# Performance work log

Hardware: AMD Instinct MI355X
Metric: run time of the kernel (lower is better)

The kernel has to match this reference:

```python
import jax, jax.numpy as jnp
import numpy as np
import math

B, S, D, H = 2, 2048, 1024, 16
HD = D // H  # head_dim = 64

def setup_inputs() -> dict:
    key = jax.random.key(0)
    ks = jax.random.split(key, 11)
    def n(k, shape, scale=1.0):
        return jax.random.normal(k, shape, dtype=jnp.float32) * scale
    w_scale = 1.0 / math.sqrt(D)
    return {
        "q": n(ks[0], (B, S, D)),
        "k": n(ks[1], (B, S, D)),
        "v": n(ks[2], (B, S, D)),
        "WQ_w": n(ks[3], (D, D), w_scale),
        "WQ_b": n(ks[4], (D,), 0.01),
        "WK_w": n(ks[5], (D, D), w_scale),
        "WK_b": n(ks[6], (D,), 0.01),
        "WV_w": n(ks[7], (D, D), w_scale),
        "WV_b": n(ks[8], (D,), 0.01),
        "Wout_w": n(ks[9], (D, D), w_scale),
        "Wout_b": n(ks[10], (D,), 0.01),
    }

def reference(q, k, v, WQ_w, WQ_b, WK_w, WK_b, WV_w, WV_b, Wout_w, Wout_b):
    b, s, _ = k.shape
    # QKV projections (torch Linear: x @ W.T + b; here weights stored [in, out])
    qh = (q @ WQ_w + WQ_b).reshape(b, -1, H, HD).transpose(0, 2, 1, 3)  # [b,h,s,hd]
    kh = (k @ WK_w + WK_b).reshape(b, -1, H, HD).transpose(0, 2, 1, 3)
    vh = (v @ WV_w + WV_b).reshape(b, -1, H, HD).transpose(0, 2, 1, 3)
    # naive attention: full [b,h,s,s] score matrix
    scores = jnp.einsum("bhqd,bhkd->bhqk", qh, kh) / math.sqrt(HD)
    attn = jax.nn.softmax(scores, axis=-1)
    out = jnp.einsum("bhqk,bhkd->bhqd", attn, vh)
    concat = out.transpose(0, 2, 1, 3).reshape(b, -1, H * HD)  # [b,s,inner_dim]
    return concat @ Wout_w + Wout_b
```

## Files before the change

kernel.cpp:

```cpp
#include <hip/hip_runtime.h>
#include <hip/hip_bf16.h>
#include <stdint.h>

typedef __attribute__((ext_vector_type(8))) short bf16x8;
typedef __attribute__((ext_vector_type(4))) short short4v;
typedef __attribute__((ext_vector_type(4))) float f32x4;

#define MFMA16x16x32 __builtin_amdgcn_mfma_f32_16x16x32_bf16

__device__ __forceinline__ short f2b(float f) {
  union { float f; uint32_t u; } x;
  x.f = f;
  uint32_t u = x.u;
  uint32_t r = (u + 0x7FFFu + ((u >> 16) & 1u)) >> 16;
  return (short)(uint16_t)r;
}

__device__ __forceinline__ uint32_t cvt_pk_bf16(float lo, float hi) {
  uint32_t r;
  asm volatile("v_cvt_pk_bf16_f32 %0, %1, %2" : "=v"(r) : "v"(lo), "v"(hi));
  return r;
}
__device__ __forceinline__ float exp2_fast(float x) {
  float r;
  asm volatile("v_exp_f32 %0, %1" : "=v"(r) : "v"(x));
  return r;
}
__device__ __forceinline__ bf16x8 cvt8(const float4 a, const float4 b) {
  union { uint32_t u[4]; bf16x8 v; } o;
  o.u[0] = cvt_pk_bf16(a.x, a.y);
  o.u[1] = cvt_pk_bf16(a.z, a.w);
  o.u[2] = cvt_pk_bf16(b.x, b.y);
  o.u[3] = cvt_pk_bf16(b.z, b.w);
  return o.v;
}

__device__ __forceinline__ void async_copy16(const void* g, void* l) {
  __builtin_amdgcn_global_load_lds(
      (const __attribute__((address_space(1))) void*)g,
      (__attribute__((address_space(3))) void*)l, 16, 0, 0);
}

__global__ void prep_kernel(const float* __restrict__ W0,
                            const float* __restrict__ W1,
                            const float* __restrict__ W2,
                            const float* __restrict__ W3,
                            const float* __restrict__ q,
                            const float* __restrict__ k,
                            const float* __restrict__ v,
                            short* __restrict__ Wt,
                            short* __restrict__ xq,
                            short* __restrict__ xk,
                            short* __restrict__ xv) {
  __shared__ short tile[64][72];
  const int z = blockIdx.z;
  const int t = threadIdx.x;
  if (z < 4) {
    const float* W = (z == 0) ? W0 : (z == 1) ? W1 : (z == 2) ? W2 : W3;
    short* Wo = Wt + (size_t)z * 1024 * 1024;
    const int r0 = blockIdx.y * 64;
    const int c0 = blockIdx.x * 64;
#pragma unroll
    for (int i = 0; i < 4; ++i) {
      const int lin = i * 1024 + t * 4;
      const int r = lin >> 6, c = lin & 63;
      const float4 vv = *(const float4*)&W[(size_t)(r0 + r) * 1024 + c0 + c];
      tile[r][c + 0] = f2b(vv.x);
      tile[r][c + 1] = f2b(vv.y);
      tile[r][c + 2] = f2b(vv.z);
      tile[r][c + 3] = f2b(vv.w);
    }
    __syncthreads();
#pragma unroll
    for (int i = 0; i < 2; ++i) {
      const int lin = i * 2048 + t * 8;
      const int r = lin >> 6, c = lin & 63;
      bf16x8 ov;
#pragma unroll
      for (int jj = 0; jj < 8; ++jj) ov[jj] = tile[c + jj][r];
      *(bf16x8*)&Wo[(size_t)(c0 + r) * 1024 + r0 + c] = ov;
    }
  } else {
    const float* x = (z == 4) ? q : (z == 5) ? k : v;
    short* yp = (z == 4) ? xq : (z == 5) ? xk : xv;
    const int base = (blockIdx.y * 16 + blockIdx.x) * 256 + t;
#pragma unroll
    for (int j = 0; j < 8; ++j) {
      const int i = base + j * 65536;
      const float4 a = ((const float4*)x)[2 * i];
      const float4 b = ((const float4*)x)[2 * i + 1];
      ((bf16x8*)yp)[i] = cvt8(a, b);
    }
  }
}

__launch_bounds__(256, 2)
__global__ void gemm_qkv_kernel(const short* __restrict__ A0,
                                const short* __restrict__ A1,
                                const short* __restrict__ A2,
                                const short* __restrict__ WtBase,
                                const float* __restrict__ b0,
                                const float* __restrict__ b1,
                                const float* __restrict__ b2,
                                short* __restrict__ C0,
                                short* __restrict__ C1,
                                short* __restrict__ Vt,
                                int ybase) {
  const int K = 1024;
  __shared__ short As[128 * 64];
  __shared__ short Bs[128 * 64];

  const int y = blockIdx.y + ybase;
  const short* A = (y == 0) ? A0 : (y == 1) ? A1 : A2;
  const short* Wt = WtBase + (size_t)y * 1024 * 1024;
  const float* bias = (y == 0) ? b0 : (y == 1) ? b1 : b2;

  const int tm = blockIdx.x & 31;
  const int tn = blockIdx.x >> 5;
  const int m0 = tm * 128, n0 = tn * 128;

  const int tid = threadIdx.x;
  const int lane = tid & 63;
  const int w = tid >> 6;
  const int wr = w >> 1, wc = w & 1;
  const int hi = lane >> 4, cc = lane & 15;
  const int srow = lane >> 3, schunk = lane & 7;

  f32x4 acc[4][4] = {};

  for (int kt = 0; kt < 16; ++kt) {
    const int k0 = kt * 64;
#pragma unroll
    for (int i = 0; i < 4; ++i) {
      const int ri = w * 4 + i;
      const int row = ri * 8 + srow;
      const int gch = schunk ^ (row & 7);
      async_copy16(A + (size_t)(m0 + row) * K + (k0 + gch * 8), &As[ri * 512]);
      async_copy16(Wt + (size_t)(n0 + row) * K + (k0 + gch * 8), &Bs[ri * 512]);
    }
    __syncthreads();
#pragma unroll
    for (int kk = 0; kk < 2; ++kk) {
      bf16x8 af[4], bfr[4];
#pragma unroll
      for (int x = 0; x < 4; ++x) {
        const int gch = kk * 4 + hi;
        const int rowA = wr * 64 + x * 16 + cc;
        af[x] = *(const bf16x8*)&As[rowA * 64 + ((gch ^ (rowA & 7)) << 3)];
        const int rowB = wc * 64 + x * 16 + cc;
        bfr[x] = *(const bf16x8*)&Bs[rowB * 64 + ((gch ^ (rowB & 7)) << 3)];
      }
#pragma unroll
      for (int x = 0; x < 4; ++x)
#pragma unroll
        for (int yy = 0; yy < 4; ++yy)
          acc[x][yy] = MFMA16x16x32(af[x], bfr[yy], acc[x][yy], 0, 0, 0);
    }
    __syncthreads();
  }

  short* Cout = (y == 0) ? C0 : C1;
#pragma unroll
  for (int x = 0; x < 4; ++x) {
    const int rbase = m0 + wr * 64 + x * 16 + (hi << 2);
#pragma unroll
    for (int yy = 0; yy < 4; ++yy) {
      const int col = n0 + wc * 64 + yy * 16 + cc;
      const float bv = bias[col];
      if (y == 2) {
        const int b = rbase >> 11, s = rbase & 2047;
        const int hh = col >> 6, d = col & 63;
        short4v pack;
#pragma unroll
        for (int r = 0; r < 4; ++r) pack[r] = f2b(acc[x][yy][r] + bv);
        *(short4v*)&Vt[((size_t)(b * 16 + hh) * 64 + d) * 2048 + s] = pack;
      } else {
#pragma unroll
        for (int r = 0; r < 4; ++r)
          Cout[(size_t)(rbase + r) * 1024 + col] = f2b(acc[x][yy][r] + bv);
      }
    }
  }
}

__launch_bounds__(256, 2)
__global__ void gemm_out_kernel(const short* __restrict__ A,
                                const short* __restrict__ Wt,
                                const float* __restrict__ bias,
                                float* __restrict__ C) {
  const int N = 1024, K = 1024;
  __shared__ short As[128 * 64];
  __shared__ short Bs[128 * 64];

  const int tm = blockIdx.x & 31;
  const int tn = blockIdx.x >> 5;
  const int m0 = tm * 128, n0 = tn * 128;

  const int tid = threadIdx.x;
  const int lane = tid & 63;
  const int w = tid >> 6;
  const int wr = w >> 1, wc = w & 1;
  const int hi = lane >> 4, cc = lane & 15;
  const int srow = lane >> 3, schunk = lane & 7;

  f32x4 acc[4][4] = {};

  for (int kt = 0; kt < 16; ++kt) {
    const int k0 = kt * 64;
#pragma unroll
    for (int i = 0; i < 4; ++i) {
      const int ri = w * 4 + i;
      const int row = ri * 8 + srow;
      const int gch = schunk ^ (row & 7);
      async_copy16(A + (size_t)(m0 + row) * K + (k0 + gch * 8), &As[ri * 512]);
      async_copy16(Wt + (size_t)(n0 + row) * K + (k0 + gch * 8), &Bs[ri * 512]);
    }
    __syncthreads();
#pragma unroll
    for (int kk = 0; kk < 2; ++kk) {
      bf16x8 af[4], bfr[4];
#pragma unroll
      for (int x = 0; x < 4; ++x) {
        const int gch = kk * 4 + hi;
        const int rowA = wr * 64 + x * 16 + cc;
        af[x] = *(const bf16x8*)&As[rowA * 64 + ((gch ^ (rowA & 7)) << 3)];
        const int rowB = wc * 64 + x * 16 + cc;
        bfr[x] = *(const bf16x8*)&Bs[rowB * 64 + ((gch ^ (rowB & 7)) << 3)];
      }
#pragma unroll
      for (int x = 0; x < 4; ++x)
#pragma unroll
        for (int yy = 0; yy < 4; ++yy)
          acc[x][yy] = MFMA16x16x32(af[x], bfr[yy], acc[x][yy], 0, 0, 0);
    }
    __syncthreads();
  }

#pragma unroll
  for (int x = 0; x < 4; ++x) {
    const int rbase = m0 + wr * 64 + x * 16 + (hi << 2);
#pragma unroll
    for (int yy = 0; yy < 4; ++yy) {
      const int col = n0 + wc * 64 + yy * 16 + cc;
      const float bv = bias[col];
#pragma unroll
      for (int r = 0; r < 4; ++r)
        C[(size_t)(rbase + r) * N + col] = acc[x][yy][r] + bv;
    }
  }
}

__launch_bounds__(256, 2)
__global__ void attn_kernel(const short* __restrict__ qh,
                            const short* __restrict__ kh,
                            const short* __restrict__ Vt,
                            short* __restrict__ concat) {
  const float CL2 = 0.18033688011112042f;
  __shared__ short Ks[2][64 * 64];
  __shared__ short Vs[2][64 * 64];
  __shared__ short Ps[2][4 * 32 * 64];

  const int qb = blockIdx.x;
  const int h = blockIdx.y;
  const int b = blockIdx.z;
  const int tid = threadIdx.x, lane = tid & 63, w = tid >> 6;
  const int hi = lane >> 4, cc = lane & 15;

  const size_t rowbase = (size_t)b * 2048;
  const int q0 = qb * 128 + w * 32;

  bf16x8 qf[2][2];
#pragma unroll
  for (int aq = 0; aq < 2; ++aq)
#pragma unroll
    for (int kk = 0; kk < 2; ++kk) {
      const int col = h * 64 + kk * 32 + hi * 8;
      qf[aq][kk] =
          *(const bf16x8*)&qh[(rowbase + q0 + aq * 16 + cc) * 1024 + col];
    }

  f32x4 oacc[2][4] = {};
  float l[2] = {0.f, 0.f};
  bf16x8 vf[2][4];

  const short* Vth = Vt + (size_t)(b * 16 + h) * 64 * 2048;
  const int srow = lane >> 3, schunk = lane & 7;
  const int e0 = (cc >> 3) & 1;

  auto STAGE = [&](int tile, int buf) {
#pragma unroll
    for (int i = 0; i < 2; ++i) {
      const int ri = w * 2 + i;
      const int row = ri * 8 + srow;
      const int gch = schunk ^ (row & 7);
      async_copy16(&kh[(rowbase + tile * 64 + row) * 1024 + h * 64 + gch * 8],
                   &Ks[buf][ri * 512]);
      async_copy16(&Vth[(size_t)row * 2048 + tile * 64 + gch * 8],
                   &Vs[buf][ri * 512]);
    }
  };
  auto QK = [&](int buf, f32x4 (&sacc)[2][4]) {
#pragma unroll
    for (int kk = 0; kk < 2; ++kk) {
      bf16x8 kf[4];
#pragma unroll
      for (int n = 0; n < 4; ++n) {
        const int row = n * 16 + cc;
        const int ch = (kk * 4 + hi) ^ (cc & 7);
        kf[n] = *(const bf16x8*)&Ks[buf][row * 64 + (ch << 3)];
      }
#pragma unroll
      for (int aq = 0; aq < 2; ++aq)
#pragma unroll
        for (int n = 0; n < 4; ++n)
          sacc[aq][n] = MFMA16x16x32(kf[n], qf[aq][kk], sacc[aq][n], 0, 0, 0);
    }
  };
  auto LOADV = [&](int buf) {
#pragma unroll
    for (int kvh = 0; kvh < 2; ++kvh) {
      const int ch = (kvh * 4 + hi) ^ (cc & 7);
#pragma unroll
      for (int n = 0; n < 4; ++n)
        vf[kvh][n] =
            *(const bf16x8*)&Vs[buf][(n * 16 + cc) * 64 + (ch << 3)];
    }
  };
  auto SOFTMAX = [&](f32x4 (&sacc)[2][4], int slot) {
    short* Pp = &Ps[slot][w * 2048];
#pragma unroll
    for (int aq = 0; aq < 2; ++aq) {
      const int qrow = aq * 16 + cc;
#pragma unroll
      for (int n = 0; n < 4; ++n) {
        const float p0 = exp2_fast(sacc[aq][n][0] * CL2);
        const float p1 = exp2_fast(sacc[aq][n][1] * CL2);
        const float p2 = exp2_fast(sacc[aq][n][2] * CL2);
        const float p3 = exp2_fast(sacc[aq][n][3] * CL2);
        l[aq] += (p0 + p1) + (p2 + p3);
        const uint32_t u0 = cvt_pk_bf16(p0, p1);
        const uint32_t u1 = cvt_pk_bf16(p2, p3);
        const int chunk = (2 * n + (hi >> 1)) ^ (cc & 7);
        const int base = qrow * 64 + (chunk << 3) + ((hi & 1) << 2);
        *(uint32_t*)&Pp[base + (e0 << 1)] = e0 ? u1 : u0;
        *(uint32_t*)&Pp[base + ((e0 ^ 1) << 1)] = e0 ? u0 : u1;
      }
    }
  };
  auto PV = [&](int slot) {
    const short* Pp = &Ps[slot][w * 2048];
#pragma unroll
    for (int kvh = 0; kvh < 2; ++kvh) {
      const int ch = (kvh * 4 + hi) ^ (cc & 7);
      bf16x8 pf[2];
#pragma unroll
      for (int aq = 0; aq < 2; ++aq)
        pf[aq] = *(const bf16x8*)&Pp[(aq * 16 + cc) * 64 + (ch << 3)];
#pragma unroll
      for (int aq = 0; aq < 2; ++aq)
#pragma unroll
        for (int n = 0; n < 4; ++n)
          oacc[aq][n] = MFMA16x16x32(vf[kvh][n], pf[aq], oacc[aq][n], 0, 0, 0);
    }
  };

  STAGE(0, 0);
  __syncthreads();
  {
    STAGE(1, 1);
    f32x4 sacc[2][4] = {};
    QK(0, sacc);
    LOADV(0);
    SOFTMAX(sacc, 0);
    __syncthreads();
  }

  for (int t = 1; t < 32; ++t) {
    const int cur = t & 1;
    if (t + 1 < 32) STAGE(t + 1, cur ^ 1);
    f32x4 sacc[2][4] = {};
    QK(cur, sacc);
    PV(cur ^ 1);
    LOADV(cur);
    SOFTMAX(sacc, cur);
    __syncthreads();
  }
  PV(1);

#pragma unroll
  for (int aq = 0; aq < 2; ++aq) {
    float lv = l[aq];
    lv += __shfl_xor(lv, 16);
    lv += __shfl_xor(lv, 32);
    const float inv = 1.0f / lv;
    const size_t grow = rowbase + q0 + aq * 16 + cc;
#pragma unroll
    for (int n = 0; n < 4; ++n)
#pragma unroll
      for (int r = 0; r < 4; ++r) {
        const int d = n * 16 + hi * 4 + r;
        concat[grow * 1024 + h * 64 + d] = f2b(oacc[aq][n][r] * inv);
      }
  }
}

extern "C" void kernel_launch(void* const* d_in, const int* in_sizes, int n_in,
                              void* d_out, int out_size, void* d_ws, size_t ws_size,
                              hipStream_t stream) {
  const float* q = (const float*)d_in[0];
  const float* k = (const float*)d_in[1];
  const float* v = (const float*)d_in[2];
  const float* WQ = (const float*)d_in[3];
  const float* bQ = (const float*)d_in[4];
  const float* WK = (const float*)d_in[5];
  const float* bK = (const float*)d_in[6];
  const float* WV = (const float*)d_in[7];
  const float* bV = (const float*)d_in[8];
  const float* WO = (const float*)d_in[9];
  const float* bO = (const float*)d_in[10];

  char* ws = (char*)d_ws;
  const size_t MB = 1024 * 1024;
  short* Wt = (short*)ws;
  short* xq = (short*)(ws + 8 * MB);
  short* xk = (short*)(ws + 16 * MB);
  short* xv = (short*)(ws + 24 * MB);
  short* qh = (short*)(ws + 32 * MB);
  short* kh = (short*)(ws + 40 * MB);
  short* concat = xk;

  prep_kernel<<<dim3(16, 16, 7), 256, 0, stream>>>(WQ, WK, WV, WO, q, k, v,
                                                   Wt, xq, xk, xv);

  if (ws_size >= 56 * MB) {
    short* Vt = (short*)(ws + 48 * MB);
    gemm_qkv_kernel<<<dim3(256, 3), 256, 0, stream>>>(
        xq, xk, xv, Wt, bQ, bK, bV, qh, kh, Vt, 0);
    attn_kernel<<<dim3(16, 16, 2), 256, 0, stream>>>(qh, kh, Vt, concat);
  } else {
    short* Vt = xq;
    gemm_qkv_kernel<<<dim3(256, 2), 256, 0, stream>>>(
        xq, xk, xv, Wt, bQ, bK, bV, qh, kh, Vt, 0);
    gemm_qkv_kernel<<<dim3(256, 1), 256, 0, stream>>>(
        xq, xk, xv, Wt, bQ, bK, bV, qh, kh, Vt, 2);
    attn_kernel<<<dim3(16, 16, 2), 256, 0, stream>>>(qh, kh, Vt, concat);
  }

  gemm_out_kernel<<<256, 256, 0, stream>>>(concat, Wt + 3 * MB, bO,
                                           (float*)d_out);
}
```

Measured before the change: 123.3 us.

## Keep softmax probabilities in registers by permuting K rows to match MFMA layout

Removes the shared-memory P buffer. The QK^T accumulator output is reused directly as the B operand of the PV MFMA, by permuting which K rows each lane loads so the score layout matches the operand layout that PV expects. The K staging swizzle is changed to stay consistent with the new row permutation. This removes the LDS writes and reads of P and a chunk of shared memory per block, at the cost of more live registers (pu array) and a more intricate index mapping.

```diff
diff --git a/kernel.cpp b/kernel.cpp
--- a/kernel.cpp
+++ b/kernel.cpp
@@ -258,7 +258,6 @@
   const float CL2 = 0.18033688011112042f;
   __shared__ short Ks[2][64 * 64];
   __shared__ short Vs[2][64 * 64];
-  __shared__ short Ps[2][4 * 32 * 64];
 
   const int qb = blockIdx.x;
   const int h = blockIdx.y;
@@ -282,20 +281,22 @@
   f32x4 oacc[2][4] = {};
   float l[2] = {0.f, 0.f};
   bf16x8 vf[2][4];
+  uint32_t pu[2][4][2];
 
   const short* Vth = Vt + (size_t)(b * 16 + h) * 64 * 2048;
   const int srow = lane >> 3, schunk = lane & 7;
-  const int e0 = (cc >> 3) & 1;
+  const int fKr = (((cc >> 2) & 1) << 2) | (cc & 3);
 
   auto STAGE = [&](int tile, int buf) {
 #pragma unroll
     for (int i = 0; i < 2; ++i) {
       const int ri = w * 2 + i;
       const int row = ri * 8 + srow;
-      const int gch = schunk ^ (row & 7);
-      async_copy16(&kh[(rowbase + tile * 64 + row) * 1024 + h * 64 + gch * 8],
+      const int gchK = schunk ^ ((((ri) & 1) << 2) | (srow & 3));
+      const int gchV = schunk ^ (row & 7);
+      async_copy16(&kh[(rowbase + tile * 64 + row) * 1024 + h * 64 + gchK * 8],
                    &Ks[buf][ri * 512]);
-      async_copy16(&Vth[(size_t)row * 2048 + tile * 64 + gch * 8],
+      async_copy16(&Vth[(size_t)row * 2048 + tile * 64 + gchV * 8],
                    &Vs[buf][ri * 512]);
     }
   };
@@ -305,8 +306,9 @@
       bf16x8 kf[4];
 #pragma unroll
       for (int n = 0; n < 4; ++n) {
-        const int row = n * 16 + cc;
-        const int ch = (kk * 4 + hi) ^ (cc & 7);
+        const int row = ((n >> 1) << 5) + (((cc >> 2)) << 3) + ((n & 1) << 2) +
+                        (cc & 3);
+        const int ch = (kk * 4 + hi) ^ fKr;
         kf[n] = *(const bf16x8*)&Ks[buf][row * 64 + (ch << 3)];
       }
 #pragma unroll
@@ -326,11 +328,9 @@
             *(const bf16x8*)&Vs[buf][(n * 16 + cc) * 64 + (ch << 3)];
     }
   };
-  auto SOFTMAX = [&](f32x4 (&sacc)[2][4], int slot) {
-    short* Pp = &Ps[slot][w * 2048];
-#pragma unroll
-    for (int aq = 0; aq < 2; ++aq) {
-      const int qrow = aq * 16 + cc;
+  auto SOFTMAX = [&](f32x4 (&sacc)[2][4]) {
+#pragma unroll
+    for (int aq = 0; aq < 2; ++aq)
 #pragma unroll
       for (int n = 0; n < 4; ++n) {
         const float p0 = exp2_fast(sacc[aq][n][0] * CL2);
@@ -338,30 +338,24 @@
         const float p2 = exp2_fast(sacc[aq][n][2] * CL2);
         const float p3 = exp2_fast(sacc[aq][n][3] * CL2);
         l[aq] += (p0 + p1) + (p2 + p3);
-        const uint32_t u0 = cvt_pk_bf16(p0, p1);
-        const uint32_t u1 = cvt_pk_bf16(p2, p3);
-        const int chunk = (2 * n + (hi >> 1)) ^ (cc & 7);
-        const int base = qrow * 64 + (chunk << 3) + ((hi & 1) << 2);
-        *(uint32_t*)&Pp[base + (e0 << 1)] = e0 ? u1 : u0;
-        *(uint32_t*)&Pp[base + ((e0 ^ 1) << 1)] = e0 ? u0 : u1;
-      }
-    }
+        pu[aq][n][0] = cvt_pk_bf16(p0, p1);
+        pu[aq][n][1] = cvt_pk_bf16(p2, p3);
+      }
   };
-  auto PV = [&](int slot) {
-    const short* Pp = &Ps[slot][w * 2048];
-#pragma unroll
-    for (int kvh = 0; kvh < 2; ++kvh) {
-      const int ch = (kvh * 4 + hi) ^ (cc & 7);
-      bf16x8 pf[2];
-#pragma unroll
-      for (int aq = 0; aq < 2; ++aq)
-        pf[aq] = *(const bf16x8*)&Pp[(aq * 16 + cc) * 64 + (ch << 3)];
-#pragma unroll
-      for (int aq = 0; aq < 2; ++aq)
+  auto PV = [&]() {
+#pragma unroll
+    for (int kvh = 0; kvh < 2; ++kvh)
+#pragma unroll
+      for (int aq = 0; aq < 2; ++aq) {
+        union { uint32_t u[4]; bf16x8 v; } pf;
+        pf.u[0] = pu[aq][2 * kvh][0];
+        pf.u[1] = pu[aq][2 * kvh][1];
+        pf.u[2] = pu[aq][2 * kvh + 1][0];
+        pf.u[3] = pu[aq][2 * kvh + 1][1];
 #pragma unroll
         for (int n = 0; n < 4; ++n)
-          oacc[aq][n] = MFMA16x16x32(vf[kvh][n], pf[aq], oacc[aq][n], 0, 0, 0);
-    }
+          oacc[aq][n] = MFMA16x16x32(vf[kvh][n], pf.v, oacc[aq][n], 0, 0, 0);
+      }
   };
 
   STAGE(0, 0);
@@ -371,7 +365,7 @@
     f32x4 sacc[2][4] = {};
     QK(0, sacc);
     LOADV(0);
-    SOFTMAX(sacc, 0);
+    SOFTMAX(sacc);
     __syncthreads();
   }
 
@@ -380,12 +374,12 @@
     if (t + 1 < 32) STAGE(t + 1, cur ^ 1);
     f32x4 sacc[2][4] = {};
     QK(cur, sacc);
-    PV(cur ^ 1);
+    PV();
     LOADV(cur);
-    SOFTMAX(sacc, cur);
-    __syncthreads();
-  }
-  PV(1);
+    SOFTMAX(sacc);
+    __syncthreads();
+  }
+  PV();
 
 #pragma unroll
   for (int aq = 0; aq < 2; ++aq) {
```

Result: faster. 115.8 us (-6.1%).
